# Performance work log

Hardware: AMD Instinct MI355X
Metric: run time of the kernel (lower is better)

## Reference

```python
import jax, jax.numpy as jnp
import numpy as np

BS, HS, IN_DIM, OUT_DIM = 256, 512, 64, 4


def setup_inputs() -> dict:
    key = jax.random.key(0)
    ks = jax.random.split(key, 14)
    u = lambda k, shp, s: s * jax.random.uniform(k, shp, dtype=jnp.float32)
    n = lambda k, shp: jax.random.normal(k, shp, dtype=jnp.float32)
    # Linear layers: PyTorch default init ~ U(-1/sqrt(fan_in), 1/sqrt(fan_in)); plain uniform is fine for a reference.
    bi_s = 1.0 / np.sqrt(IN_DIM)
    bh_s = 1.0 / np.sqrt(HS)
    return {
        "inputs": n(ks[0], (BS, IN_DIM)),
        "hidden": n(ks[1], (BS, HS)),
        "hebb": n(ks[2], (BS, HS, HS)),
        "Wi": u(ks[3], (HS, IN_DIM), bi_s),   # i2h weight
        "bi": u(ks[4], (HS,), bi_s),
        "w": 0.01 * jax.random.uniform(ks[5], (HS, HS), dtype=jnp.float32),      # fixed recurrent weights
        "alpha": 0.01 * jax.random.uniform(ks[6], (HS, HS), dtype=jnp.float32),  # plasticity coefficients
        "Wo": u(ks[7], (OUT_DIM, HS), bh_s),  # h2o
        "bo": u(ks[8], (OUT_DIM,), bh_s),
        "Wv": u(ks[9], (1, HS), bh_s),        # h2v
        "bv": u(ks[10], (1,), bh_s),
        "Wda": u(ks[11], (1, HS), bh_s),      # h2DA
        "bda": u(ks[12], (1,), bh_s),
    }


def reference(inputs, hidden, hebb, Wi, bi, w, alpha, Wo, bo, Wv, bv, Wda, bda):
    # hactiv = tanh(i2h(x) + (w + alpha*hebb) @ hidden)
    rec = hidden @ w.T + jnp.einsum("ij,bij,bj->bi", alpha, hebb, hidden)  # [B,HS]
    hactiv = jnp.tanh(inputs @ Wi.T + bi + rec)                              # [B,HS]
    activout = hactiv @ Wo.T + bo                                            # [B,OUT]
    valueout = hactiv @ Wv.T + bv                                            # [B,1]
    DAout = jnp.tanh(hactiv @ Wda.T + bda)                                   # [B,1] (da='tanh')
    # deltahebb = outer(hactiv, hidden); fm=1 -> fully DA-modulated update
    deltahebb = hactiv[:, :, None] * hidden[:, None, :]                      # [B,HS,HS]
    hebb_new = jnp.clip(hebb + DAout[:, :, None] * deltahebb, -1.0, 1.0)
    return activout, valueout, DAout, hactiv, hebb_new
```

## Files before the change

### kernel.cpp

```cpp
#include <hip/hip_runtime.h>

#define BS 256
#define HS 512
#define IN_DIM 64
#define OUT_DIM 4

typedef float nfloat4 __attribute__((ext_vector_type(4)));

__global__ __launch_bounds__(256) void rec_kernel(
    const float* __restrict__ hidden,
    const float* __restrict__ hebb,
    const float* __restrict__ w,
    const float* __restrict__ alpha,
    float* __restrict__ rec)
{
    const int wid  = blockIdx.x * 4 + (threadIdx.x >> 6);
    const int lane = threadIdx.x & 63;
    const int row0 = wid * 2;
    const int b  = row0 >> 9;
    const int i0 = row0 & (HS - 1);

    const float4* __restrict__ hebb40 = (const float4*)(hebb + (size_t)row0 * HS);
    const float4* __restrict__ hebb41 = hebb40 + HS / 4;
    const float4* __restrict__ w40    = (const float4*)(w     + (size_t)i0 * HS);
    const float4* __restrict__ w41    = w40 + HS / 4;
    const float4* __restrict__ a40    = (const float4*)(alpha + (size_t)i0 * HS);
    const float4* __restrict__ a41    = a40 + HS / 4;
    const float4* __restrict__ h4     = (const float4*)(hidden + (size_t)b * HS);

    const float4 hh0 = h4[lane];
    const float4 hh1 = h4[lane + 64];

    const float4 hbA0 = hebb40[lane];
    const float4 hbA1 = hebb40[lane + 64];
    const float4 hbB0 = hebb41[lane];
    const float4 hbB1 = hebb41[lane + 64];
    const float4 wwA0 = w40[lane];
    const float4 wwA1 = w40[lane + 64];
    const float4 wwB0 = w41[lane];
    const float4 wwB1 = w41[lane + 64];
    const float4 aaA0 = a40[lane];
    const float4 aaA1 = a40[lane + 64];
    const float4 aaB0 = a41[lane];
    const float4 aaB1 = a41[lane + 64];

    float sA = 0.f, sB = 0.f;
    sA += hh0.x * (wwA0.x + aaA0.x * hbA0.x);
    sA += hh0.y * (wwA0.y + aaA0.y * hbA0.y);
    sA += hh0.z * (wwA0.z + aaA0.z * hbA0.z);
    sA += hh0.w * (wwA0.w + aaA0.w * hbA0.w);
    sA += hh1.x * (wwA1.x + aaA1.x * hbA1.x);
    sA += hh1.y * (wwA1.y + aaA1.y * hbA1.y);
    sA += hh1.z * (wwA1.z + aaA1.z * hbA1.z);
    sA += hh1.w * (wwA1.w + aaA1.w * hbA1.w);

    sB += hh0.x * (wwB0.x + aaB0.x * hbB0.x);
    sB += hh0.y * (wwB0.y + aaB0.y * hbB0.y);
    sB += hh0.z * (wwB0.z + aaB0.z * hbB0.z);
    sB += hh0.w * (wwB0.w + aaB0.w * hbB0.w);
    sB += hh1.x * (wwB1.x + aaB1.x * hbB1.x);
    sB += hh1.y * (wwB1.y + aaB1.y * hbB1.y);
    sB += hh1.z * (wwB1.z + aaB1.z * hbB1.z);
    sB += hh1.w * (wwB1.w + aaB1.w * hbB1.w);

#pragma unroll
    for (int off = 32; off > 0; off >>= 1) {
        sA += __shfl_xor(sA, off, 64);
        sB += __shfl_xor(sB, off, 64);
    }
    if (lane == 0) {
        rec[row0]     = sA;
        rec[row0 + 1] = sB;
    }
}

__global__ __launch_bounds__(512) void act_kernel(
    const float* __restrict__ inputs,
    const float* __restrict__ Wi, const float* __restrict__ bi,
    const float* __restrict__ rec,
    const float* __restrict__ Wo, const float* __restrict__ bo,
    const float* __restrict__ Wv, const float* __restrict__ bv,
    const float* __restrict__ Wda, const float* __restrict__ bda,
    float* __restrict__ activout, float* __restrict__ valueout,
    float* __restrict__ daout, float* __restrict__ hactiv,
    float* __restrict__ scale)
{
    const int b = blockIdx.x;
    const int i = threadIdx.x;

    __shared__ __align__(16) float sh_in[IN_DIM];
    __shared__ float red[8][8];
    __shared__ float da_sh;

    if (i < IN_DIM) sh_in[i] = inputs[b * IN_DIM + i];
    __syncthreads();

    float dot = 0.f;
    const float4* __restrict__ wi4 = (const float4*)(Wi + (size_t)i * IN_DIM);
    const float4* __restrict__ in4 = (const float4*)sh_in;
#pragma unroll
    for (int t = 0; t < IN_DIM / 4; ++t) {
        const float4 a = wi4[t];
        const float4 x = in4[t];
        dot += a.x * x.x + a.y * x.y + a.z * x.z + a.w * x.w;
    }

    const float h = tanhf(dot + bi[i] + rec[(size_t)b * HS + i]);
    hactiv[(size_t)b * HS + i] = h;

    float p[6];
    p[0] = h * Wo[0 * HS + i];
    p[1] = h * Wo[1 * HS + i];
    p[2] = h * Wo[2 * HS + i];
    p[3] = h * Wo[3 * HS + i];
    p[4] = h * Wv[i];
    p[5] = h * Wda[i];

    const int lane = i & 63, wave = i >> 6;
#pragma unroll
    for (int k = 0; k < 6; ++k) {
        float s = p[k];
#pragma unroll
        for (int off = 32; off > 0; off >>= 1)
            s += __shfl_xor(s, off, 64);
        if (lane == 0) red[wave][k] = s;
    }
    __syncthreads();

    if (i < 6) {
        float s = 0.f;
#pragma unroll
        for (int wv = 0; wv < 8; ++wv) s += red[wv][i];
        if (i < 4) {
            activout[b * OUT_DIM + i] = s + bo[i];
        } else if (i == 4) {
            valueout[b] = s + bv[0];
        } else {
            const float da = tanhf(s + bda[0]);
            daout[b] = da;
            da_sh = da;
        }
    }
    __syncthreads();

    scale[(size_t)b * HS + i] = da_sh * h;
}

__global__ __launch_bounds__(256) void hebb_kernel(
    const float* __restrict__ hebb,
    const float* __restrict__ hidden,
    const float* __restrict__ scale,
    float* __restrict__ hebb_new)
{
    const long long total4 = (long long)BS * HS * HS / 4;
    const long long stride = (long long)gridDim.x * blockDim.x;
    const long long tid    = (long long)blockIdx.x * blockDim.x + threadIdx.x;

#pragma unroll
    for (int k = 0; k < 16; k += 2) {
        const long long vA = total4 - 1 - tid - (long long)k * stride;
        const long long vB = vA - stride;

        const long long eA = vA * 4;
        const int bA = (int)(eA >> 18);
        const int iA = (int)(eA >> 9) & (HS - 1);
        const int jA = (int)eA & (HS - 1);
        const long long eB = vB * 4;
        const int bB = (int)(eB >> 18);
        const int iB = (int)(eB >> 9) & (HS - 1);
        const int jB = (int)eB & (HS - 1);

        const float4 hbA = ((const float4*)hebb)[vA];
        const float4 hbB = ((const float4*)hebb)[vB];
        const float  sAs = scale[bA * HS + iA];
        const float4 hiA = *(const float4*)(hidden + bA * HS + jA);
        const float  sBs = scale[bB * HS + iB];
        const float4 hiB = *(const float4*)(hidden + bB * HS + jB);

        nfloat4 oA, oB;
        oA.x = fminf(fmaxf(hbA.x + sAs * hiA.x, -1.f), 1.f);
        oA.y = fminf(fmaxf(hbA.y + sAs * hiA.y, -1.f), 1.f);
        oA.z = fminf(fmaxf(hbA.z + sAs * hiA.z, -1.f), 1.f);
        oA.w = fminf(fmaxf(hbA.w + sAs * hiA.w, -1.f), 1.f);
        oB.x = fminf(fmaxf(hbB.x + sBs * hiB.x, -1.f), 1.f);
        oB.y = fminf(fmaxf(hbB.y + sBs * hiB.y, -1.f), 1.f);
        oB.z = fminf(fmaxf(hbB.z + sBs * hiB.z, -1.f), 1.f);
        oB.w = fminf(fmaxf(hbB.w + sBs * hiB.w, -1.f), 1.f);
        __builtin_nontemporal_store(oA, (nfloat4*)hebb_new + vA);
        __builtin_nontemporal_store(oB, (nfloat4*)hebb_new + vB);
    }
}

extern "C" void kernel_launch(void* const* d_in, const int* in_sizes, int n_in,
                              void* d_out, int out_size, void* d_ws, size_t ws_size,
                              hipStream_t stream) {
    const float* inputs = (const float*)d_in[0];
    const float* hidden = (const float*)d_in[1];
    const float* hebb   = (const float*)d_in[2];
    const float* Wi     = (const float*)d_in[3];
    const float* bi     = (const float*)d_in[4];
    const float* w      = (const float*)d_in[5];
    const float* alpha  = (const float*)d_in[6];
    const float* Wo     = (const float*)d_in[7];
    const float* bo     = (const float*)d_in[8];
    const float* Wv     = (const float*)d_in[9];
    const float* bv     = (const float*)d_in[10];
    const float* Wda    = (const float*)d_in[11];
    const float* bda    = (const float*)d_in[12];

    float* out = (float*)d_out;
    float* activout = out;
    float* valueout = out + 1024;
    float* daout    = out + 1280;
    float* hactiv   = out + 1536;
    float* hebb_new = out + 1536 + BS * HS;

    float* rec   = (float*)d_ws;
    float* scale = rec;

    rec_kernel<<<(BS * HS) / 8, 256, 0, stream>>>(hidden, hebb, w, alpha, rec);

    act_kernel<<<BS, HS, 0, stream>>>(inputs, Wi, bi, rec, Wo, bo, Wv, bv,
                                      Wda, bda, activout, valueout, daout,
                                      hactiv, scale);

    hebb_kernel<<<4096, 256, 0, stream>>>(hebb, hidden, scale, hebb_new);
}
```

Baseline: 138.6 us.

## Split batch into two halves so hebb stays cache-resident between kernels

Runs the rec, act and hebb kernels twice, once per half of the batch, passing a batch offset to each kernel. The hebb kernel now walks its half forward instead of walking the whole tensor in reverse. The aim is that each 128MB half of hebb, after being read by rec_kernel, is still in the last-level cache when hebb_kernel reads it again. This avoids a second full read from HBM. The cost is twice as many kernel launches with smaller grids, and less parallelism in each launch.

```diff
diff --git a/kernel.cpp b/kernel.cpp
--- a/kernel.cpp
+++ b/kernel.cpp
@@ -4,6 +4,7 @@
 #define HS 512
 #define IN_DIM 64
 #define OUT_DIM 4
+#define HALF_BS 128
 
 typedef float nfloat4 __attribute__((ext_vector_type(4)));
 
@@ -12,11 +13,12 @@
     const float* __restrict__ hebb,
     const float* __restrict__ w,
     const float* __restrict__ alpha,
-    float* __restrict__ rec)
+    float* __restrict__ rec,
+    int b_base)
 {
     const int wid  = blockIdx.x * 4 + (threadIdx.x >> 6);
     const int lane = threadIdx.x & 63;
-    const int row0 = wid * 2;
+    const int row0 = b_base * HS + wid * 2;
     const int b  = row0 >> 9;
     const int i0 = row0 & (HS - 1);
 
@@ -83,9 +85,10 @@
     const float* __restrict__ Wda, const float* __restrict__ bda,
     float* __restrict__ activout, float* __restrict__ valueout,
     float* __restrict__ daout, float* __restrict__ hactiv,
-    float* __restrict__ scale)
+    float* __restrict__ scale,
+    int b_base)
 {
-    const int b = blockIdx.x;
+    const int b = b_base + blockIdx.x;
     const int i = threadIdx.x;
 
     __shared__ __align__(16) float sh_in[IN_DIM];
@@ -150,16 +153,17 @@
     const float* __restrict__ hebb,
     const float* __restrict__ hidden,
     const float* __restrict__ scale,
-    float* __restrict__ hebb_new)
+    float* __restrict__ hebb_new,
+    int b_base)
 {
-    const long long total4 = (long long)BS * HS * HS / 4;
+    const long long half_base = (long long)b_base * HS * HS / 4;
     const long long stride = (long long)gridDim.x * blockDim.x;
     const long long tid    = (long long)blockIdx.x * blockDim.x + threadIdx.x;
 
 #pragma unroll
     for (int k = 0; k < 16; k += 2) {
-        const long long vA = total4 - 1 - tid - (long long)k * stride;
-        const long long vB = vA - stride;
+        const long long vA = half_base + tid + (long long)k * stride;
+        const long long vB = vA + stride;
 
         const long long eA = vA * 4;
         const int bA = (int)(eA >> 18);
@@ -218,11 +222,13 @@
     float* rec   = (float*)d_ws;
     float* scale = rec;
 
-    rec_kernel<<<(BS * HS) / 8, 256, 0, stream>>>(hidden, hebb, w, alpha, rec);
-
-    act_kernel<<<BS, HS, 0, stream>>>(inputs, Wi, bi, rec, Wo, bo, Wv, bv,
-                                      Wda, bda, activout, valueout, daout,
-                                      hactiv, scale);
-
-    hebb_kernel<<<4096, 256, 0, stream>>>(hebb, hidden, scale, hebb_new);
-}
+    for (int c = 0; c < 2; ++c) {
+        const int b_base = c * HALF_BS;
+        rec_kernel<<<(HALF_BS * HS) / 8, 256, 0, stream>>>(hidden, hebb, w, alpha,
+                                                           rec, b_base);
+        act_kernel<<<HALF_BS, HS, 0, stream>>>(inputs, Wi, bi, rec, Wo, bo, Wv, bv,
+                                               Wda, bda, activout, valueout, daout,
+                                               hactiv, scale, b_base);
+        hebb_kernel<<<2048, 256, 0, stream>>>(hebb, hidden, scale, hebb_new, b_base);
+    }
+}
```

New measurement: 149.9 us. +8.2%, slower.
